# Performance work log

Measured on AMD Instinct MI355X. Metric: run time of the kernel, lower is better.

The kernel has to match this reference:

```python
import jax, jax.numpy as jnp
import numpy as np

B = 131072      # batch
D_IN = 256      # cfg.input_dim
H = 512         # hidden width
D_OUT = 128     # cfg.output_dim
ALPHA = 0.2     # cfg.alpha
EPS = 1e-6      # cfg.eps
K_MAX = 1000    # cfg.k_max


def _init_linear(k, shape, fan_in):
    lim = 1.0 / np.sqrt(fan_in)
    return jax.random.uniform(k, shape, jnp.float32, -lim, lim)


def setup_inputs() -> dict:
    key = jax.random.key(0)
    ks = jax.random.split(key, 7)
    return {
        "x": jax.random.normal(ks[0], (B, D_IN), jnp.float32),
        "W1": _init_linear(ks[1], (D_IN, H), D_IN),
        "b1": _init_linear(ks[2], (H,), D_IN),
        "W2": _init_linear(ks[3], (H, H), H),
        "b2": _init_linear(ks[4], (H,), H),
        "W3": _init_linear(ks[5], (H, D_OUT), H),
        "b3": _init_linear(ks[6], (D_OUT,), H),
    }


def _mlp(x, W1, b1, W2, b2, W3, b3):
    # MLP with tanh activations (cfg.act_F='tanh'), final layer linear
    h = jnp.tanh(x @ W1 + b1)
    h = jnp.tanh(h @ W2 + b2)
    return h @ W3 + b3  # (B, D_OUT)


def _fixed_point(F_x):
    # y_{k+1} = y_k + alpha * tanh(F_x - y_k); break when max_b ||y_{k+1}-y_k||_2 < eps
    y0 = jnp.zeros_like(F_x)

    def cond(state):
        y, k, done = state
        return (k < K_MAX) & (~done)

    def body(state):
        y, k, done = state
        y_next = y + ALPHA * jnp.tanh(F_x - y)
        step = jnp.sqrt(jnp.sum(jnp.square(y_next - y), axis=1))  # (B,)
        done = jnp.max(step) < EPS
        return (y_next, k + 1, done)

    y, _, _ = jax.lax.while_loop(cond, body, (y0, jnp.int32(0), jnp.bool_(False)))
    return y


def reference(x, W1, b1, W2, b2, W3, b3):
    F_x = _mlp(x, W1, b1, W2, b2, W3, b3)
    return _fixed_point(F_x)
```

## Files before the change

### kernel.cpp

```cpp
#include <hip/hip_runtime.h>

typedef short s16x8 __attribute__((ext_vector_type(8)));
typedef unsigned short u16x8 __attribute__((ext_vector_type(8)));
typedef float f32x16 __attribute__((ext_vector_type(16)));

__device__ __forceinline__ unsigned short f2bf(float f) {
  unsigned u = __float_as_uint(f);
  u += 0x7fffu + ((u >> 16) & 1u);
  return (unsigned short)(u >> 16);
}

__device__ __forceinline__ float tanh_fast(float x) {
  float xc = fminf(15.f, fmaxf(-15.f, x));
  float t = __builtin_amdgcn_exp2f(xc * 2.8853900817779268f);
  return (t - 1.f) * __builtin_amdgcn_rcpf(t + 1.f);
}

__global__ __launch_bounds__(256)
void prep_pack(const float* __restrict__ W1, const float* __restrict__ W2,
               const float* __restrict__ W3, unsigned short* __restrict__ ws) {
  __shared__ unsigned short t[64][65];
  const int b = blockIdx.x;
  const float* W; unsigned short* base; int KK, N, tk, tn;
  if (b < 32)      { W = W1; base = ws;          KK = 16; N = 512; tk = b >> 3;       tn = b & 7; }
  else if (b < 96) { int g = b - 32; W = W2; base = ws + 131072; KK = 32; N = 512; tk = g >> 3; tn = g & 7; }
  else             { int g = b - 96; W = W3; base = ws + 393216; KK = 32; N = 128; tk = g >> 1; tn = g & 1; }

  const int tid = threadIdx.x;
  #pragma unroll
  for (int p = 0; p < 16; ++p) {
    int kl = p * 4 + (tid >> 6);
    int nl = tid & 63;
    t[kl][nl] = f2bf(W[(size_t)(tk * 64 + kl) * N + tn * 64 + nl]);
  }
  __syncthreads();

  const int lane = tid & 63, ln31 = lane & 31, khalf = lane >> 5;
  #pragma unroll
  for (int pass = 0; pass < 2; ++pass) {
    int pair = pass * 4 + (tid >> 6);
    int tn_l = pair & 1, kk_l = pair >> 1;
    int tile = tn * 2 + tn_l, kk = tk * 4 + kk_l;
    u16x8 v;
    #pragma unroll
    for (int j = 0; j < 8; ++j)
      v[j] = t[kk_l * 16 + khalf * 8 + j][tn_l * 32 + ln31];
    *(u16x8*)(base + ((size_t)(tile * KK + kk) * 64 + lane) * 8) = v;
  }
}

#define LDSIDX(ch, row) (((ch) << 9) + ((((row) + (ch)) & 63) << 3))

__global__ __launch_bounds__(512, 4)
void mlp_limit_kernel(const float* __restrict__ x,
                      const float* __restrict__ b1, const float* __restrict__ b2,
                      const float* __restrict__ b3,
                      const unsigned short* __restrict__ w1p,
                      const unsigned short* __restrict__ w2p,
                      const unsigned short* __restrict__ w3p,
                      float* __restrict__ out) {
  __shared__ __align__(16) unsigned short lds[64 * 512];
  const int tid   = threadIdx.x;
  const int w     = tid >> 6;
  const int lane  = tid & 63;
  const int ln31  = lane & 31;
  const int khalf = lane >> 5;
  const int m0    = blockIdx.x * 64;

  #pragma unroll
  for (int c = tid; c < 2048; c += 512) {
    int row = c >> 5, ch = c & 31;
    const float4* src = (const float4*)(x + (size_t)(m0 + row) * 256 + ch * 8);
    float4 f0 = src[0], f1 = src[1];
    u16x8 v;
    v[0] = f2bf(f0.x); v[1] = f2bf(f0.y); v[2] = f2bf(f0.z); v[3] = f2bf(f0.w);
    v[4] = f2bf(f1.x); v[5] = f2bf(f1.y); v[6] = f2bf(f1.z); v[7] = f2bf(f1.w);
    *(u16x8*)&lds[LDSIDX(ch, row)] = v;
  }
  __syncthreads();

  const int ncb = w * 64;

  f32x16 acc[2][2];
  #pragma unroll
  for (int mt = 0; mt < 2; ++mt)
    #pragma unroll
    for (int nt = 0; nt < 2; ++nt)
      #pragma unroll
      for (int r = 0; r < 16; ++r) acc[mt][nt][r] = 0.f;

  {
    const s16x8* b0p = (const s16x8*)w1p + (size_t)(w * 2) * 16 * 64 + lane;
    const s16x8* b1p = b0p + 16 * 64;
    #pragma unroll 2
    for (int kk = 0; kk < 16; ++kk) {
      int ch = kk * 2 + khalf;
      s16x8 a0 = *(const s16x8*)&lds[LDSIDX(ch, ln31)];
      s16x8 a1 = *(const s16x8*)&lds[LDSIDX(ch, 32 + ln31)];
      s16x8 b0 = b0p[kk * 64];
      s16x8 b1 = b1p[kk * 64];
      acc[0][0] = __builtin_amdgcn_mfma_f32_32x32x16_bf16(a0, b0, acc[0][0], 0, 0, 0);
      acc[0][1] = __builtin_amdgcn_mfma_f32_32x32x16_bf16(a0, b1, acc[0][1], 0, 0, 0);
      acc[1][0] = __builtin_amdgcn_mfma_f32_32x32x16_bf16(a1, b0, acc[1][0], 0, 0, 0);
      acc[1][1] = __builtin_amdgcn_mfma_f32_32x32x16_bf16(a1, b1, acc[1][1], 0, 0, 0);
    }
  }
  __syncthreads();

  {
    float bias[2];
    bias[0] = b1[ncb + ln31];
    bias[1] = b1[ncb + 32 + ln31];
    #pragma unroll
    for (int mt = 0; mt < 2; ++mt)
      #pragma unroll
      for (int nt = 0; nt < 2; ++nt) {
        int hc = ncb + nt * 32 + ln31;
        int chh = hc >> 3, wi = hc & 7;
        #pragma unroll
        for (int r = 0; r < 16; ++r) {
          int m = mt * 32 + (r & 3) + 8 * (r >> 2) + 4 * khalf;
          lds[(chh << 9) + (((m + chh) & 63) << 3) + wi] =
              f2bf(tanh_fast(acc[mt][nt][r] + bias[nt]));
        }
      }
  }
  __syncthreads();

  #pragma unroll
  for (int mt = 0; mt < 2; ++mt)
    #pragma unroll
    for (int nt = 0; nt < 2; ++nt)
      #pragma unroll
      for (int r = 0; r < 16; ++r) acc[mt][nt][r] = 0.f;

  {
    const s16x8* b0p = (const s16x8*)w2p + (size_t)(w * 2) * 32 * 64 + lane;
    const s16x8* b1p = b0p + 32 * 64;
    #pragma unroll 2
    for (int kk = 0; kk < 32; ++kk) {
      int ch = kk * 2 + khalf;
      s16x8 a0 = *(const s16x8*)&lds[LDSIDX(ch, ln31)];
      s16x8 a1 = *(const s16x8*)&lds[LDSIDX(ch, 32 + ln31)];
      s16x8 b0 = b0p[kk * 64];
      s16x8 b1 = b1p[kk * 64];
      acc[0][0] = __builtin_amdgcn_mfma_f32_32x32x16_bf16(a0, b0, acc[0][0], 0, 0, 0);
      acc[0][1] = __builtin_amdgcn_mfma_f32_32x32x16_bf16(a0, b1, acc[0][1], 0, 0, 0);
      acc[1][0] = __builtin_amdgcn_mfma_f32_32x32x16_bf16(a1, b0, acc[1][0], 0, 0, 0);
      acc[1][1] = __builtin_amdgcn_mfma_f32_32x32x16_bf16(a1, b1, acc[1][1], 0, 0, 0);
    }
  }
  __syncthreads();

  {
    float bias[2];
    bias[0] = b2[ncb + ln31];
    bias[1] = b2[ncb + 32 + ln31];
    #pragma unroll
    for (int mt = 0; mt < 2; ++mt)
      #pragma unroll
      for (int nt = 0; nt < 2; ++nt) {
        int hc = ncb + nt * 32 + ln31;
        int chh = hc >> 3, wi = hc & 7;
        #pragma unroll
        for (int r = 0; r < 16; ++r) {
          int m = mt * 32 + (r & 3) + 8 * (r >> 2) + 4 * khalf;
          lds[(chh << 9) + (((m + chh) & 63) << 3) + wi] =
              f2bf(tanh_fast(acc[mt][nt][r] + bias[nt]));
        }
      }
  }
  __syncthreads();

  {
    f32x16 acc3;
    #pragma unroll
    for (int r = 0; r < 16; ++r) acc3[r] = 0.f;
    const int mb = (w & 1) * 32;
    const int t3 = w >> 1;
    const s16x8* bp = (const s16x8*)w3p + (size_t)t3 * 32 * 64 + lane;
    #pragma unroll 2
    for (int kk = 0; kk < 32; ++kk) {
      int ch = kk * 2 + khalf;
      s16x8 a = *(const s16x8*)&lds[LDSIDX(ch, mb + ln31)];
      s16x8 b = bp[kk * 64];
      acc3 = __builtin_amdgcn_mfma_f32_32x32x16_bf16(a, b, acc3, 0, 0, 0);
    }
    float bz = b3[t3 * 32 + ln31];
    #pragma unroll
    for (int r = 0; r < 16; ++r) {
      int m = m0 + mb + (r & 3) + 8 * (r >> 2) + 4 * khalf;
      out[(size_t)m * 128 + t3 * 32 + ln31] = acc3[r] + bz;
    }
  }
}

extern "C" void kernel_launch(void* const* d_in, const int* in_sizes, int n_in,
                              void* d_out, int out_size, void* d_ws, size_t ws_size,
                              hipStream_t stream) {
  const float* x  = (const float*)d_in[0];
  const float* W1 = (const float*)d_in[1];
  const float* b1 = (const float*)d_in[2];
  const float* W2 = (const float*)d_in[3];
  const float* b2 = (const float*)d_in[4];
  const float* W3 = (const float*)d_in[5];
  const float* b3 = (const float*)d_in[6];
  float* out = (float*)d_out;
  unsigned short* ws = (unsigned short*)d_ws;

  hipLaunchKernelGGL(prep_pack, dim3(112), dim3(256), 0, stream, W1, W2, W3, ws);
  hipLaunchKernelGGL(mlp_limit_kernel, dim3(2048), dim3(512), 0, stream,
                     x, b1, b2, b3, ws, ws + 131072, ws + 393216, out);
}
```

Measured before the change: 383.5 us.

## Switch LDS to row-major XOR swizzle and software-pipeline MFMA operand loads

Replaces the chunk-major rotated LDS layout with a row-major layout that XOR-swizzles 16-byte chunks by row, and rewrites the epilogue stores and A-fragment reads to use precomputed base offsets. The MFMA loops are fully unrolled with double-buffered A (LDS) and B (global) fragments prefetched one and two steps ahead, so load latency can hide behind matrix instructions. The layer-3 wave-to-tile mapping changes and the wave index is marked uniform. Full unrolling and the extra buffers raise register pressure, which may be a concern under the 4-blocks-per-CU launch bound.

```diff
diff --git a/kernel.cpp b/kernel.cpp
--- a/kernel.cpp
+++ b/kernel.cpp
@@ -49,7 +49,7 @@
   }
 }
 
-#define LDSIDX(ch, row) (((ch) << 9) + ((((row) + (ch)) & 63) << 3))
+#define ABASE(row) ((row) * 512 + ((row) & 7) * 8)
 
 __global__ __launch_bounds__(512, 4)
 void mlp_limit_kernel(const float* __restrict__ x,
@@ -61,7 +61,7 @@
                       float* __restrict__ out) {
   __shared__ __align__(16) unsigned short lds[64 * 512];
   const int tid   = threadIdx.x;
-  const int w     = tid >> 6;
+  const int w     = __builtin_amdgcn_readfirstlane(tid >> 6);
   const int lane  = tid & 63;
   const int ln31  = lane & 31;
   const int khalf = lane >> 5;
@@ -75,121 +75,139 @@
     u16x8 v;
     v[0] = f2bf(f0.x); v[1] = f2bf(f0.y); v[2] = f2bf(f0.z); v[3] = f2bf(f0.w);
     v[4] = f2bf(f1.x); v[5] = f2bf(f1.y); v[6] = f2bf(f1.z); v[7] = f2bf(f1.w);
-    *(u16x8*)&lds[LDSIDX(ch, row)] = v;
-  }
-  __syncthreads();
-
-  const int ncb = w * 64;
+    *(u16x8*)&lds[row * 512 + ((ch ^ (row & 7)) * 8)] = v;
+  }
+  __syncthreads();
+
+  const int abase0 = ABASE(ln31);
+  const int abase1 = ABASE(ln31 + 32);
+  const int ncb    = w * 64;
+  const int kh32   = khalf * 32;
+  const int khA    = khalf * 8;
 
   f32x16 acc[2][2];
+
   #pragma unroll
   for (int mt = 0; mt < 2; ++mt)
     #pragma unroll
     for (int nt = 0; nt < 2; ++nt)
       #pragma unroll
       for (int r = 0; r < 16; ++r) acc[mt][nt][r] = 0.f;
-
   {
-    const s16x8* b0p = (const s16x8*)w1p + (size_t)(w * 2) * 16 * 64 + lane;
-    const s16x8* b1p = b0p + 16 * 64;
-    #pragma unroll 2
+    const s16x8* bp0 = (const s16x8*)w1p + (size_t)((w * 2 + 0) * 16) * 64 + lane;
+    const s16x8* bp1 = (const s16x8*)w1p + (size_t)((w * 2 + 1) * 16) * 64 + lane;
+    s16x8 a0[2], a1[2], b0[2], b1[2];
+    b0[0] = bp0[0];  b1[0] = bp1[0];
+    b0[1] = bp0[64]; b1[1] = bp1[64];
+    a0[0] = *(const s16x8*)&lds[abase0 ^ khA];
+    a1[0] = *(const s16x8*)&lds[abase1 ^ khA];
+    #pragma unroll
     for (int kk = 0; kk < 16; ++kk) {
-      int ch = kk * 2 + khalf;
-      s16x8 a0 = *(const s16x8*)&lds[LDSIDX(ch, ln31)];
-      s16x8 a1 = *(const s16x8*)&lds[LDSIDX(ch, 32 + ln31)];
-      s16x8 b0 = b0p[kk * 64];
-      s16x8 b1 = b1p[kk * 64];
-      acc[0][0] = __builtin_amdgcn_mfma_f32_32x32x16_bf16(a0, b0, acc[0][0], 0, 0, 0);
-      acc[0][1] = __builtin_amdgcn_mfma_f32_32x32x16_bf16(a0, b1, acc[0][1], 0, 0, 0);
-      acc[1][0] = __builtin_amdgcn_mfma_f32_32x32x16_bf16(a1, b0, acc[1][0], 0, 0, 0);
-      acc[1][1] = __builtin_amdgcn_mfma_f32_32x32x16_bf16(a1, b1, acc[1][1], 0, 0, 0);
-    }
-  }
-  __syncthreads();
-
+      const int s = kk & 1, d = s ^ 1;
+      if (kk + 1 < 16) {
+        a0[d] = *(const s16x8*)&lds[abase0 ^ ((kk + 1) * 16 + khA)];
+        a1[d] = *(const s16x8*)&lds[abase1 ^ ((kk + 1) * 16 + khA)];
+      }
+      acc[0][0] = __builtin_amdgcn_mfma_f32_32x32x16_bf16(a0[s], b0[s], acc[0][0], 0, 0, 0);
+      acc[0][1] = __builtin_amdgcn_mfma_f32_32x32x16_bf16(a0[s], b1[s], acc[0][1], 0, 0, 0);
+      acc[1][0] = __builtin_amdgcn_mfma_f32_32x32x16_bf16(a1[s], b0[s], acc[1][0], 0, 0, 0);
+      acc[1][1] = __builtin_amdgcn_mfma_f32_32x32x16_bf16(a1[s], b1[s], acc[1][1], 0, 0, 0);
+      if (kk + 2 < 16) {
+        b0[s] = bp0[(kk + 2) * 64];
+        b1[s] = bp1[(kk + 2) * 64];
+      }
+    }
+  }
+  __syncthreads();
+
+  #pragma unroll
+  for (int nt = 0; nt < 2; ++nt) {
+    int hc = ncb + nt * 32 + ln31;
+    float bias = b1[hc];
+    int wi = hc & 7;
+    int e  = (((hc >> 3) * 8) ^ kh32) + wi + khalf * 2048;
+    #pragma unroll
+    for (int mt = 0; mt < 2; ++mt)
+      #pragma unroll
+      for (int r = 0; r < 16; ++r) {
+        int C = (mt * 32 + (r & 3) + 8 * (r >> 2)) * 512;
+        lds[C + (e ^ ((r & 3) * 8))] = f2bf(tanh_fast(acc[mt][nt][r] + bias));
+      }
+  }
+  __syncthreads();
+
+  #pragma unroll
+  for (int mt = 0; mt < 2; ++mt)
+    #pragma unroll
+    for (int nt = 0; nt < 2; ++nt)
+      #pragma unroll
+      for (int r = 0; r < 16; ++r) acc[mt][nt][r] = 0.f;
   {
-    float bias[2];
-    bias[0] = b1[ncb + ln31];
-    bias[1] = b1[ncb + 32 + ln31];
+    const s16x8* bp0 = (const s16x8*)w2p + (size_t)((w * 2 + 0) * 32) * 64 + lane;
+    const s16x8* bp1 = (const s16x8*)w2p + (size_t)((w * 2 + 1) * 32) * 64 + lane;
+    s16x8 a0[2], a1[2], b0[2], b1[2];
+    b0[0] = bp0[0];  b1[0] = bp1[0];
+    b0[1] = bp0[64]; b1[1] = bp1[64];
+    a0[0] = *(const s16x8*)&lds[abase0 ^ khA];
+    a1[0] = *(const s16x8*)&lds[abase1 ^ khA];
+    #pragma unroll
+    for (int kk = 0; kk < 32; ++kk) {
+      const int s = kk & 1, d = s ^ 1;
+      if (kk + 1 < 32) {
+        a0[d] = *(const s16x8*)&lds[abase0 ^ ((kk + 1) * 16 + khA)];
+        a1[d] = *(const s16x8*)&lds[abase1 ^ ((kk + 1) * 16 + khA)];
+      }
+      acc[0][0] = __builtin_amdgcn_mfma_f32_32x32x16_bf16(a0[s], b0[s], acc[0][0], 0, 0, 0);
+      acc[0][1] = __builtin_amdgcn_mfma_f32_32x32x16_bf16(a0[s], b1[s], acc[0][1], 0, 0, 0);
+      acc[1][0] = __builtin_amdgcn_mfma_f32_32x32x16_bf16(a1[s], b0[s], acc[1][0], 0, 0, 0);
+      acc[1][1] = __builtin_amdgcn_mfma_f32_32x32x16_bf16(a1[s], b1[s], acc[1][1], 0, 0, 0);
+      if (kk + 2 < 32) {
+        b0[s] = bp0[(kk + 2) * 64];
+        b1[s] = bp1[(kk + 2) * 64];
+      }
+    }
+  }
+  __syncthreads();
+
+  #pragma unroll
+  for (int nt = 0; nt < 2; ++nt) {
+    int hc = ncb + nt * 32 + ln31;
+    float bias = b2[hc];
+    int wi = hc & 7;
+    int e  = (((hc >> 3) * 8) ^ kh32) + wi + khalf * 2048;
     #pragma unroll
     for (int mt = 0; mt < 2; ++mt)
       #pragma unroll
-      for (int nt = 0; nt < 2; ++nt) {
-        int hc = ncb + nt * 32 + ln31;
-        int chh = hc >> 3, wi = hc & 7;
-        #pragma unroll
-        for (int r = 0; r < 16; ++r) {
-          int m = mt * 32 + (r & 3) + 8 * (r >> 2) + 4 * khalf;
-          lds[(chh << 9) + (((m + chh) & 63) << 3) + wi] =
-              f2bf(tanh_fast(acc[mt][nt][r] + bias[nt]));
-        }
-      }
-  }
-  __syncthreads();
-
-  #pragma unroll
-  for (int mt = 0; mt < 2; ++mt)
-    #pragma unroll
-    for (int nt = 0; nt < 2; ++nt)
-      #pragma unroll
-      for (int r = 0; r < 16; ++r) acc[mt][nt][r] = 0.f;
+      for (int r = 0; r < 16; ++r) {
+        int C = (mt * 32 + (r & 3) + 8 * (r >> 2)) * 512;
+        lds[C + (e ^ ((r & 3) * 8))] = f2bf(tanh_fast(acc[mt][nt][r] + bias));
+      }
+  }
+  __syncthreads();
 
   {
-    const s16x8* b0p = (const s16x8*)w2p + (size_t)(w * 2) * 32 * 64 + lane;
-    const s16x8* b1p = b0p + 32 * 64;
-    #pragma unroll 2
+    const int mh  = (w >> 2) * 32;
+    const int t3  = w & 3;
+    const int ab  = ABASE(mh + ln31);
+    f32x16 acc3;
+    #pragma unroll
+    for (int r = 0; r < 16; ++r) acc3[r] = 0.f;
+    const s16x8* bp = (const s16x8*)w3p + (size_t)(t3 * 32) * 64 + lane;
+    s16x8 a[2], b[2];
+    b[0] = bp[0]; b[1] = bp[64];
+    a[0] = *(const s16x8*)&lds[ab ^ khA];
+    #pragma unroll
     for (int kk = 0; kk < 32; ++kk) {
-      int ch = kk * 2 + khalf;
-      s16x8 a0 = *(const s16x8*)&lds[LDSIDX(ch, ln31)];
-      s16x8 a1 = *(const s16x8*)&lds[LDSIDX(ch, 32 + ln31)];
-      s16x8 b0 = b0p[kk * 64];
-      s16x8 b1 = b1p[kk * 64];
-      acc[0][0] = __builtin_amdgcn_mfma_f32_32x32x16_bf16(a0, b0, acc[0][0], 0, 0, 0);
-      acc[0][1] = __builtin_amdgcn_mfma_f32_32x32x16_bf16(a0, b1, acc[0][1], 0, 0, 0);
-      acc[1][0] = __builtin_amdgcn_mfma_f32_32x32x16_bf16(a1, b0, acc[1][0], 0, 0, 0);
-      acc[1][1] = __builtin_amdgcn_mfma_f32_32x32x16_bf16(a1, b1, acc[1][1], 0, 0, 0);
-    }
-  }
-  __syncthreads();
-
-  {
-    float bias[2];
-    bias[0] = b2[ncb + ln31];
-    bias[1] = b2[ncb + 32 + ln31];
-    #pragma unroll
-    for (int mt = 0; mt < 2; ++mt)
-      #pragma unroll
-      for (int nt = 0; nt < 2; ++nt) {
-        int hc = ncb + nt * 32 + ln31;
-        int chh = hc >> 3, wi = hc & 7;
-        #pragma unroll
-        for (int r = 0; r < 16; ++r) {
-          int m = mt * 32 + (r & 3) + 8 * (r >> 2) + 4 * khalf;
-          lds[(chh << 9) + (((m + chh) & 63) << 3) + wi] =
-              f2bf(tanh_fast(acc[mt][nt][r] + bias[nt]));
-        }
-      }
-  }
-  __syncthreads();
-
-  {
-    f32x16 acc3;
-    #pragma unroll
-    for (int r = 0; r < 16; ++r) acc3[r] = 0.f;
-    const int mb = (w & 1) * 32;
-    const int t3 = w >> 1;
-    const s16x8* bp = (const s16x8*)w3p + (size_t)t3 * 32 * 64 + lane;
-    #pragma unroll 2
-    for (int kk = 0; kk < 32; ++kk) {
-      int ch = kk * 2 + khalf;
-      s16x8 a = *(const s16x8*)&lds[LDSIDX(ch, mb + ln31)];
-      s16x8 b = bp[kk * 64];
-      acc3 = __builtin_amdgcn_mfma_f32_32x32x16_bf16(a, b, acc3, 0, 0, 0);
+      const int s = kk & 1, d = s ^ 1;
+      if (kk + 1 < 32)
+        a[d] = *(const s16x8*)&lds[ab ^ ((kk + 1) * 16 + khA)];
+      acc3 = __builtin_amdgcn_mfma_f32_32x32x16_bf16(a[s], b[s], acc3, 0, 0, 0);
+      if (kk + 2 < 32) b[s] = bp[(kk + 2) * 64];
     }
     float bz = b3[t3 * 32 + ln31];
     #pragma unroll
     for (int r = 0; r < 16; ++r) {
-      int m = m0 + mb + (r & 3) + 8 * (r >> 2) + 4 * khalf;
+      int m = m0 + mh + (r & 3) + 8 * (r >> 2) + 4 * khalf;
       out[(size_t)m * 128 + t3 * 32 + ln31] = acc3[r] + bz;
     }
   }
```

New measurement: 328.9 us. 1.17x faster.
